# Optimization experiments

Hardware: AMD Instinct MI355X
Metric: run time of the kernel (lower is better)

Reference implementation:

```python
import jax, jax.numpy as jnp
import numpy as np

V = 20000; FV = 2000; PV = 31
SE = 400; FE = 50; PE = 5; NE = 5
FR = FE + PE + NE  # 60, field_rep_embed_size
H = 512; HH = H // 2  # decoder hidden, encoder per-direction hidden
B = 32; T = 32; S = 100
TE = 300  # target_lookup dim (hardcoded in module)


def setup_inputs() -> dict:
    key = jax.random.key(0)
    ks = jax.random.split(key, 26)
    g = lambda k, shape, s: (jax.random.normal(k, shape, jnp.float32) * s)
    inp = {}
    inp['sent'] = jax.random.randint(ks[0], (B, T), 0, V)
    inp['value'] = jax.random.randint(ks[1], (B, S), 0, V)
    inp['field'] = jax.random.randint(ks[2], (B, S), 0, FV)
    inp['ppos'] = jax.random.randint(ks[3], (B, S), 0, PV)
    inp['pneg'] = jax.random.randint(ks[4], (B, S), 0, PV)
    inp['batch_size'] = B
    inp['value_mask'] = jnp.ones((B, S), jnp.float32)
    inp['align_prob'] = jax.random.uniform(ks[5], (B, S, V), jnp.float32)
    # embedding tables
    inp['sent_emb'] = g(ks[6], (V, SE), 0.05)
    inp['field_emb'] = g(ks[7], (FV, FE), 0.05)
    inp['ppos_emb'] = g(ks[8], (PV, PE), 0.05)
    inp['pneg_emb'] = g(ks[9], (PV, NE), 0.05)
    inp['target_emb'] = g(ks[10], (V, TE), 0.05)
    # bidirectional encoder LSTM (per-direction hidden HH), torch gate order i,f,g,o
    ein = SE + FR
    inp['Wi_f'] = g(ks[11], (ein, 4 * HH), ein ** -0.5)
    inp['Wh_f'] = g(ks[12], (HH, 4 * HH), HH ** -0.5)
    inp['b_f'] = jnp.zeros((4 * HH,), jnp.float32)
    inp['Wi_b'] = g(ks[13], (ein, 4 * HH), ein ** -0.5)
    inp['Wh_b'] = g(ks[14], (HH, 4 * HH), HH ** -0.5)
    inp['b_b'] = jnp.zeros((4 * HH,), jnp.float32)
    # decoder LSTM cell + dual attention params
    inp['Wi_d'] = g(ks[15], (SE, 4 * H), SE ** -0.5)
    inp['Wh_d'] = g(ks[16], (H, 4 * H), H ** -0.5)
    inp['b_d'] = jnp.zeros((4 * H,), jnp.float32)
    inp['Wa'] = g(ks[17], (H, H), H ** -0.5)   # encoder-state attention proj
    inp['Wf'] = g(ks[18], (FR, H), FR ** -0.5) # field-rep attention proj
    inp['Wo'] = g(ks[19], (2 * H, H), (2 * H) ** -0.5)  # output proj [h;ctx]
    inp['Wl'] = g(ks[20], (2 * H + SE, 1), (2 * H + SE) ** -0.5)  # lamda gate
    inp['bl'] = jnp.zeros((1,), jnp.float32)
    # linear_out: encoder_hidden_size -> vocab
    inp['Wout'] = g(ks[21], (H, V), H ** -0.5)
    inp['bout'] = jnp.zeros((V,), jnp.float32)
    return inp


def _cell(x, h, c, Wi, Wh, b):
    z = x @ Wi + h @ Wh + b
    i, f, g, o = jnp.split(z, 4, axis=-1)
    c = jax.nn.sigmoid(f) * c + jax.nn.sigmoid(i) * jnp.tanh(g)
    h = jax.nn.sigmoid(o) * jnp.tanh(c)
    return h, c


def _run_lstm(xseq, Wi, Wh, b):
    # xseq [B,L,E] -> hs [B,L,Hn], (hT, cT)
    Bn = xseq.shape[0]; Hn = Wh.shape[0]
    init = (jnp.zeros((Bn, Hn), xseq.dtype), jnp.zeros((Bn, Hn), xseq.dtype))
    def step(carry, xt):
        h, c = _cell(xt, carry[0], carry[1], Wi, Wh, b)
        return (h, c), h
    (hT, cT), hs = jax.lax.scan(step, init, jnp.swapaxes(xseq, 0, 1))
    return jnp.swapaxes(hs, 0, 1), hT, cT


def reference(sent, value, field, ppos, pneg, batch_size, value_mask, align_prob,
              sent_emb, field_emb, ppos_emb, pneg_emb, target_emb,
              Wi_f, Wh_f, b_f, Wi_b, Wh_b, b_b,
              Wi_d, Wh_d, b_d, Wa, Wf, Wo, Wl, bl, Wout, bout):
    # --- encoder input: word emb of table values + field/pos/neg-pos embs ---
    input_d = sent_emb[value]                                     # [B,S,SE]
    input_z = jnp.concatenate([field_emb[field], ppos_emb[ppos], pneg_emb[pneg]], axis=2)  # [B,S,FR]
    enc_in = jnp.concatenate([input_d, input_z], axis=2)          # [B,S,SE+FR]
    # bidirectional LSTM (dropout is eval-mode identity)
    hs_f, hTf, cTf = _run_lstm(enc_in, Wi_f, Wh_f, b_f)
    hs_b, hTb, cTb = _run_lstm(enc_in[:, ::-1], Wi_b, Wh_b, b_b)
    enc_out = jnp.concatenate([hs_f, hs_b[:, ::-1]], axis=-1)     # [B,S,H]
    h0 = jnp.concatenate([hTf, hTb], axis=-1)                     # [B,H]
    c0 = jnp.concatenate([cTf, cTb], axis=-1)

    # --- dual-attention decoder ---
    x_seq = sent_emb[sent]                                        # [B,T,SE]
    enc_proj = jnp.einsum('bsh,hk->bsk', enc_out, Wa)             # word-level keys
    z_proj = jnp.einsum('bsf,fk->bsk', input_z, Wf)               # field-level keys

    def dstep(carry, xt):
        h, c = _cell(xt, carry[0], carry[1], Wi_d, Wh_d, b_d)
        alpha = jax.nn.softmax(jnp.einsum('bsh,bh->bs', enc_proj, h), axis=-1)
        beta = jax.nn.softmax(jnp.einsum('bsh,bh->bs', z_proj, h), axis=-1)
        g = alpha * beta
        g = g / (jnp.sum(g, axis=-1, keepdims=True) + 1e-9)       # dual attn weights
        ctx = jnp.einsum('bs,bsh->bh', g, enc_out)
        out = jnp.tanh(jnp.concatenate([h, ctx], axis=-1) @ Wo)   # [B,H]
        lam = jax.nn.sigmoid(jnp.concatenate([h, ctx, xt], axis=-1) @ Wl + bl)  # [B,1]
        return (h, c), (out, g, lam)

    (hT, cT), (outs, attn, lam) = jax.lax.scan(dstep, (h0, c0), jnp.swapaxes(x_seq, 0, 1))
    outs = jnp.swapaxes(outs, 0, 1)   # [B,T,H]
    attn = jnp.swapaxes(attn, 0, 1)   # [B,T,S]
    lam = jnp.swapaxes(lam, 0, 1)     # [B,T,1]

    p_mod = jax.nn.log_softmax(outs @ Wout + bout, axis=2)        # [B,T,V]
    p_lex = jnp.einsum('bts,bsv->btv', attn, align_prob)          # bmm
    p_bias = jax.nn.log_softmax(lam * p_lex + (1.0 - lam) * p_mod, axis=2)

    # position_idx_to_value: vectorized gather replacing the scalar double loop
    max_idx_attn = jnp.argmax(attn, axis=2)                       # [B,T]
    word_idx = jnp.take_along_axis(value, max_idx_attn, axis=1)   # [B,T]
    attn_pred = target_emb[word_idx]                              # [B,T,300]
    decoder_pred = target_emb[jnp.argmax(p_bias, axis=2)]         # [B,T,300]
    return p_bias, (hT, cT), attn_pred, decoder_pred
```

## Files before the change

### kernel.cpp

```cpp
#include <hip/hip_runtime.h>
#include <cstdint>
#include <cstddef>

static constexpr int Bn  = 32;
static constexpr int Tn  = 32;
static constexpr int Sn  = 100;
static constexpr int Vn  = 20000;
static constexpr int SEn = 400;
static constexpr int EINn= 460;
static constexpr int Hn  = 512;
static constexpr int HHn = 256;
static constexpr int TEn = 300;

__device__ __forceinline__ float sigm(float x) { return 1.f / (1.f + expf(-x)); }

__device__ __forceinline__ void fma4(float hk, const float4 w,
                                     float& zi, float& zf, float& zg, float& zo) {
    zi = fmaf(hk, w.x, zi); zf = fmaf(hk, w.y, zf);
    zg = fmaf(hk, w.z, zg); zo = fmaf(hk, w.w, zo);
}

__device__ __forceinline__ void grid_wait(int* bar, int target) {
    while (__hip_atomic_load(bar, __ATOMIC_ACQUIRE, __HIP_MEMORY_SCOPE_AGENT) < target)
        __builtin_amdgcn_s_sleep(2);
}

__global__ __launch_bounds__(256) void embed_kernel(
    const int* __restrict__ value, const int* __restrict__ field,
    const int* __restrict__ ppos, const int* __restrict__ pneg,
    const int* __restrict__ sent,
    const float* __restrict__ sent_emb, const float* __restrict__ field_emb,
    const float* __restrict__ ppos_emb, const float* __restrict__ pneg_emb,
    float* __restrict__ enc_in, float* __restrict__ x_seq)
{
    int i = blockIdx.x * 256 + threadIdx.x;
    const int total1 = Bn * Sn * EINn;
    if (i < total1) {
        int e = i % EINn, bs = i / EINn;
        float v;
        if (e < SEn)      v = sent_emb[(size_t)value[bs] * SEn + e];
        else if (e < 450) v = field_emb[field[bs] * 50 + (e - 400)];
        else if (e < 455) v = ppos_emb[ppos[bs] * 5 + (e - 450)];
        else              v = pneg_emb[pneg[bs] * 5 + (e - 455)];
        enc_in[i] = v;
    } else {
        int i2 = i - total1;
        if (i2 < Bn * Tn * SEn) {
            int e = i2 % SEn, bt = i2 / SEn;
            x_seq[i2] = sent_emb[(size_t)sent[bt] * SEn + e];
        }
    }
}

__global__ __launch_bounds__(256) void transpose_wh_kernel(
    const float* __restrict__ Whf, const float* __restrict__ Whb,
    const float* __restrict__ Whd,
    float* __restrict__ Whf_t, float* __restrict__ Whb_t, float* __restrict__ Whd_t)
{
    int i = blockIdx.x * 256 + threadIdx.x;
    if (i < 65536) {
        int k = i >> 8, u = i & 255;
        const float* p = Whf + (size_t)k * 1024 + u;
        float4 o;
        o.x = p[0]; o.y = p[256]; o.z = p[512]; o.w = p[768];
        *(float4*)(Whf_t + (size_t)i * 4) = o;
        p = Whb + (size_t)k * 1024 + u;
        o.x = p[0]; o.y = p[256]; o.z = p[512]; o.w = p[768];
        *(float4*)(Whb_t + (size_t)i * 4) = o;
    } else {
        int j = i - 65536;
        if (j < 262144) {
            int k = j >> 9, u = j & 511;
            const float* p = Whd + (size_t)k * 2048 + u;
            float4 o;
            o.x = p[0]; o.y = p[512]; o.z = p[1024]; o.w = p[1536];
            *(float4*)(Whd_t + (size_t)j * 4) = o;
        }
    }
}

__global__ __launch_bounds__(256) void gemm128_kernel(
    const float* __restrict__ A, const float* __restrict__ Bm,
    const float* __restrict__ bias, float* __restrict__ C,
    int M, int N, int K, int lda, int ldb, int ldc)
{
    __shared__ float As[8][128];
    __shared__ float Bs[8][128];
    const int bm = blockIdx.y * 128, bn = blockIdx.x * 128;
    const int tid = threadIdx.x;
    const int tx = tid & 15, ty = tid >> 4;
    const int row0 = ty * 8, col0 = tx * 8;
    float acc[8][8] = {};
    for (int k0 = 0; k0 < K; k0 += 8) {
        #pragma unroll
        for (int i = 0; i < 4; ++i) {
            int idx = tid + 256 * i;
            int m = idx >> 3, kk = idx & 7;
            float v = 0.f;
            if (bm + m < M && k0 + kk < K) v = A[(size_t)(bm + m) * lda + (k0 + kk)];
            As[kk][m] = v;
        }
        #pragma unroll
        for (int i = 0; i < 4; ++i) {
            int idx = tid + 256 * i;
            int kk = idx >> 7, n = idx & 127;
            float v = 0.f;
            if (k0 + kk < K && bn + n < N) v = Bm[(size_t)(k0 + kk) * ldb + (bn + n)];
            Bs[kk][n] = v;
        }
        __syncthreads();
        #pragma unroll
        for (int kk = 0; kk < 8; ++kk) {
            float a[8], b[8];
            #pragma unroll
            for (int i = 0; i < 8; ++i) a[i] = As[kk][row0 + i];
            #pragma unroll
            for (int j = 0; j < 8; ++j) b[j] = Bs[kk][col0 + j];
            #pragma unroll
            for (int i = 0; i < 8; ++i)
                #pragma unroll
                for (int j = 0; j < 8; ++j) acc[i][j] = fmaf(a[i], b[j], acc[i][j]);
        }
        __syncthreads();
    }
    #pragma unroll
    for (int i = 0; i < 8; ++i) {
        int m = bm + row0 + i;
        if (m >= M) continue;
        #pragma unroll
        for (int j = 0; j < 8; ++j) {
            int n = bn + col0 + j;
            if (n < N) {
                float v = acc[i][j];
                if (bias) v += bias[n];
                C[(size_t)m * ldc + n] = v;
            }
        }
    }
}

__global__ __launch_bounds__(256, 1) void enc_lstm5_kernel(
    const float* __restrict__ Xf, const float* __restrict__ Xb,
    const float4* __restrict__ Whf_t, const float4* __restrict__ Whb_t,
    float* __restrict__ enc_out, float* __restrict__ h0t, float* __restrict__ c0t,
    float* __restrict__ hbuf, int* __restrict__ bar)
{
    const int bb  = blockIdx.x;
    const int dir = bb >> 5;
    const int U0  = (bb & 31) * 8;
    const float*  __restrict__ X = dir ? Xb : Xf;
    const float4* __restrict__ W = dir ? Whb_t : Whf_t;
    float* hb = hbuf + dir * 16384;
    const int tid = threadIdx.x;
    const int b = tid & 31, uu = tid >> 5;
    const int unit = U0 + uu;
    const float4* __restrict__ wcol = W + unit;
    __shared__ float h_lds[HHn * 32];
    float c = 0.f;

    for (int s = 0; s < Sn; ++s) {
        const int src_s = dir ? (Sn - 1 - s) : s;
        const float* xr = X + ((size_t)(b * Sn + src_s)) * 1024 + unit;
        float zi = xr[0], zf = xr[256], zg = xr[512], zo = xr[768];
        if (s > 0) {
            if (tid == 0) grid_wait(bar, 64 * s);
            __syncthreads();
            const float4* src4 = (const float4*)(hb + ((s - 1) & 1) * 8192);
            float4* dst4 = (float4*)h_lds;
            #pragma unroll
            for (int i = 0; i < 8; ++i)
                dst4[tid + i * 256] = src4[tid + i * 256];
            __syncthreads();
            #pragma unroll 8
            for (int k = 0; k < 256; ++k)
                fma4(h_lds[k * 32 + b], wcol[(size_t)k * 256], zi, zf, zg, zo);
        }
        c = sigm(zf) * c + sigm(zi) * tanhf(zg);
        const float h = sigm(zo) * tanhf(c);
        enc_out[((size_t)(b * Sn + src_s)) * Hn + dir * HHn + unit] = h;
        if (s == Sn - 1) {
            h0t[(dir * HHn + unit) * 32 + b] = h;
            c0t[(dir * HHn + unit) * 32 + b] = c;
        } else {
            hb[(s & 1) * 8192 + unit * 32 + b] = h;
            __syncthreads();
            if (tid == 0)
                __hip_atomic_fetch_add(bar, 1, __ATOMIC_ACQ_REL, __HIP_MEMORY_SCOPE_AGENT);
        }
    }
}

__global__ __launch_bounds__(256, 1) void dec_lstm5_kernel(
    const float* __restrict__ Xd, const float4* __restrict__ Whd_t,
    const float* __restrict__ h0t, const float* __restrict__ c0t,
    float* __restrict__ h_all, float* __restrict__ hT, float* __restrict__ cT,
    float* __restrict__ hbuf, int* __restrict__ bar)
{
    const int U0 = blockIdx.x * 8;
    const int tid = threadIdx.x;
    const int b = tid & 31, uu = tid >> 5;
    const int unit = U0 + uu;
    const float4* __restrict__ wcol = Whd_t + unit;
    __shared__ float h_lds[Hn * 32];
    float c = c0t[unit * 32 + b];

    for (int t = 0; t < Tn; ++t) {
        const float* xr = Xd + ((size_t)(b * Tn + t)) * 2048 + unit;
        float zi = xr[0], zf = xr[512], zg = xr[1024], zo = xr[1536];
        if (t > 0) {
            if (tid == 0) grid_wait(bar, 64 * t);
        }
        __syncthreads();
        const float4* src4 = (t == 0) ? (const float4*)h0t
                                      : (const float4*)(hbuf + ((t - 1) & 1) * 16384);
        float4* dst4 = (float4*)h_lds;
        #pragma unroll
        for (int i = 0; i < 16; ++i)
            dst4[tid + i * 256] = src4[tid + i * 256];
        __syncthreads();
        #pragma unroll 8
        for (int k = 0; k < 512; ++k)
            fma4(h_lds[k * 32 + b], wcol[(size_t)k * 512], zi, zf, zg, zo);
        c = sigm(zf) * c + sigm(zi) * tanhf(zg);
        const float h = sigm(zo) * tanhf(c);
        h_all[((size_t)(b * Tn + t)) * Hn + unit] = h;
        if (t == Tn - 1) {
            hT[b * Hn + unit] = h;
            cT[b * Hn + unit] = c;
        } else {
            hbuf[(t & 1) * 16384 + unit * 32 + b] = h;
            __syncthreads();
            if (tid == 0)
                __hip_atomic_fetch_add(bar, 1, __ATOMIC_ACQ_REL, __HIP_MEMORY_SCOPE_AGENT);
        }
    }
}

__global__ __launch_bounds__(256) void dec_post_kernel(
    const float* __restrict__ h_all, const float* __restrict__ enc_proj,
    const float* __restrict__ z_proj, const float* __restrict__ enc_out,
    const float* __restrict__ x_seq, const float* __restrict__ Wo,
    const float* __restrict__ Wl, const float* __restrict__ bl,
    const int* __restrict__ value, const float* __restrict__ target_emb,
    float* __restrict__ outs, float* __restrict__ gattn,
    float* __restrict__ lamv, float* __restrict__ attn_pred)
{
    const int bt = blockIdx.x, b = bt >> 5;
    const int tid = threadIdx.x;
    __shared__ float h_sh[Hn];
    __shared__ float sc[2 * Sn];
    __shared__ float g_sh[Sn];
    __shared__ float ctx_sh[Hn];
    __shared__ float red[256];
    __shared__ int smax_sh;

    for (int i = tid; i < Hn; i += 256) h_sh[i] = h_all[(size_t)bt * Hn + i];
    __syncthreads();

    const int wave = tid >> 6, lane = tid & 63;
    for (int s = wave; s < Sn; s += 4) {
        const float* ep = enc_proj + ((size_t)b * Sn + s) * Hn;
        const float* zp = z_proj  + ((size_t)b * Sn + s) * Hn;
        float da = 0.f, db = 0.f;
        for (int j = lane; j < Hn; j += 64) {
            float hv = h_sh[j];
            da = fmaf(ep[j], hv, da);
            db = fmaf(zp[j], hv, db);
        }
        #pragma unroll
        for (int off = 32; off; off >>= 1) {
            da += __shfl_down(da, off);
            db += __shfl_down(db, off);
        }
        if (lane == 0) { sc[s] = da; sc[Sn + s] = db; }
    }
    __syncthreads();

    if (tid == 0) {
        float ma = -1e30f, mb = -1e30f;
        for (int s = 0; s < Sn; ++s) { ma = fmaxf(ma, sc[s]); mb = fmaxf(mb, sc[Sn + s]); }
        float sa = 0.f, sb = 0.f;
        for (int s = 0; s < Sn; ++s) {
            float ea = expf(sc[s] - ma), eb = expf(sc[Sn + s] - mb);
            sc[s] = ea; sc[Sn + s] = eb; sa += ea; sb += eb;
        }
        float gs = 0.f;
        for (int s = 0; s < Sn; ++s) { float g = (sc[s] / sa) * (sc[Sn + s] / sb); g_sh[s] = g; gs += g; }
        float inv = 1.f / (gs + 1e-9f);
        float best = -1.f; int bi = 0;
        for (int s = 0; s < Sn; ++s) {
            float g = g_sh[s] * inv; g_sh[s] = g;
            if (g > best) { best = g; bi = s; }
        }
        smax_sh = bi;
    }
    __syncthreads();

    for (int s = tid; s < Sn; s += 256) gattn[(size_t)bt * Sn + s] = g_sh[s];
    const int word = value[b * Sn + smax_sh];
    for (int e = tid; e < TEn; e += 256)
        attn_pred[(size_t)bt * TEn + e] = target_emb[(size_t)word * TEn + e];

    for (int u = tid; u < Hn; u += 256) {
        float acc = 0.f;
        for (int s = 0; s < Sn; ++s)
            acc = fmaf(g_sh[s], enc_out[((size_t)b * Sn + s) * Hn + u], acc);
        ctx_sh[u] = acc;
    }
    __syncthreads();

    for (int j = tid; j < Hn; j += 256) {
        float acc = 0.f;
        for (int k = 0; k < Hn; ++k) acc = fmaf(h_sh[k], Wo[(size_t)k * Hn + j], acc);
        for (int k = 0; k < Hn; ++k) acc = fmaf(ctx_sh[k], Wo[(size_t)(Hn + k) * Hn + j], acc);
        outs[(size_t)bt * Hn + j] = tanhf(acc);
    }

    float part = 0.f;
    for (int k = tid; k < Hn; k += 256) part = fmaf(h_sh[k], Wl[k], part);
    for (int k = tid; k < Hn; k += 256) part = fmaf(ctx_sh[k], Wl[Hn + k], part);
    const float* xr = x_seq + (size_t)bt * SEn;
    for (int k = tid; k < SEn; k += 256) part = fmaf(xr[k], Wl[2 * Hn + k], part);
    red[tid] = part;
    __syncthreads();
    for (int s2 = 128; s2; s2 >>= 1) {
        if (tid < s2) red[tid] += red[tid + s2];
        __syncthreads();
    }
    if (tid == 0) lamv[bt] = 1.f / (1.f + expf(-(red[0] + bl[0])));
}

__global__ __launch_bounds__(256) void p_lex_kernel(
    const float* __restrict__ gattn, const float* __restrict__ align_prob,
    float* __restrict__ p_lex)
{
    const int b = blockIdx.z, th = blockIdx.y, vc = blockIdx.x;
    const int tid = threadIdx.x;
    __shared__ float gT[Sn][17];
    for (int i = tid; i < Sn * 16; i += 256) {
        int s = i >> 4, tt = i & 15;
        gT[s][tt] = gattn[((size_t)(b * Tn + th * 16 + tt)) * Sn + s];
    }
    __syncthreads();
    const int v0 = vc * 1024 + tid * 4;
    if (v0 >= Vn) return;
    float acc[16][4] = {};
    for (int s = 0; s < Sn; ++s) {
        const float4 a = *(const float4*)(align_prob + ((size_t)b * Sn + s) * Vn + v0);
        #pragma unroll
        for (int tt = 0; tt < 16; ++tt) {
            float g = gT[s][tt];
            acc[tt][0] = fmaf(g, a.x, acc[tt][0]);
            acc[tt][1] = fmaf(g, a.y, acc[tt][1]);
            acc[tt][2] = fmaf(g, a.z, acc[tt][2]);
            acc[tt][3] = fmaf(g, a.w, acc[tt][3]);
        }
    }
    #pragma unroll
    for (int tt = 0; tt < 16; ++tt) {
        float4 o;
        o.x = acc[tt][0]; o.y = acc[tt][1]; o.z = acc[tt][2]; o.w = acc[tt][3];
        *(float4*)(p_lex + ((size_t)(b * Tn + th * 16 + tt)) * Vn + v0) = o;
    }
}

__global__ __launch_bounds__(256) void reduce1_kernel(
    const float* __restrict__ z, float* __restrict__ lse1)
{
    const int r = blockIdx.x, tid = threadIdx.x;
    const float* row = z + (size_t)r * Vn;
    __shared__ float red[256];
    float m = -1e30f;
    for (int v = tid; v < Vn; v += 256) m = fmaxf(m, row[v]);
    red[tid] = m; __syncthreads();
    for (int s = 128; s; s >>= 1) { if (tid < s) red[tid] = fmaxf(red[tid], red[tid + s]); __syncthreads(); }
    m = red[0]; __syncthreads();
    float sum = 0.f;
    for (int v = tid; v < Vn; v += 256) sum += expf(row[v] - m);
    red[tid] = sum; __syncthreads();
    for (int s = 128; s; s >>= 1) { if (tid < s) red[tid] += red[tid + s]; __syncthreads(); }
    if (tid == 0) lse1[r] = m + logf(red[0]);
}

__global__ __launch_bounds__(256) void combine_kernel(
    float* __restrict__ q, const float* __restrict__ p_lex,
    const float* __restrict__ lamv, const float* __restrict__ lse1,
    float* __restrict__ lse2, int* __restrict__ amax)
{
    const int r = blockIdx.x, tid = threadIdx.x;
    const float l = lamv[r], ls1 = lse1[r];
    float* row = q + (size_t)r * Vn;
    const float* pl = p_lex + (size_t)r * Vn;
    __shared__ float rm[256];
    __shared__ int ri[256];
    float m = -1e30f; int mi = 0;
    for (int v = tid; v < Vn; v += 256) {
        float qq = l * pl[v] + (1.f - l) * (row[v] - ls1);
        row[v] = qq;
        if (qq > m) { m = qq; mi = v; }
    }
    rm[tid] = m; ri[tid] = mi; __syncthreads();
    for (int s = 128; s; s >>= 1) {
        if (tid < s) {
            if (rm[tid + s] > rm[tid] || (rm[tid + s] == rm[tid] && ri[tid + s] < ri[tid])) {
                rm[tid] = rm[tid + s]; ri[tid] = ri[tid + s];
            }
        }
        __syncthreads();
    }
    m = rm[0];
    const int best = ri[0];
    __syncthreads();
    float sum = 0.f;
    for (int v = tid; v < Vn; v += 256) sum += expf(row[v] - m);
    rm[tid] = sum; __syncthreads();
    for (int s = 128; s; s >>= 1) { if (tid < s) rm[tid] += rm[tid + s]; __syncthreads(); }
    if (tid == 0) { lse2[r] = m + logf(rm[0]); amax[r] = best; }
}

__global__ __launch_bounds__(256) void finalize_kernel(
    float* __restrict__ pbias, const float* __restrict__ lse2,
    const int* __restrict__ amax, const float* __restrict__ target_emb,
    float* __restrict__ dec_pred)
{
    const int r = blockIdx.x, tid = threadIdx.x;
    const float ls = lse2[r];
    float* row = pbias + (size_t)r * Vn;
    for (int v = tid; v < Vn; v += 256) row[v] -= ls;
    const int wd = amax[r];
    for (int e = tid; e < TEn; e += 256)
        dec_pred[(size_t)r * TEn + e] = target_emb[(size_t)wd * TEn + e];
}

extern "C" void kernel_launch(void* const* d_in, const int* in_sizes, int n_in,
                              void* d_out, int out_size, void* d_ws, size_t ws_size,
                              hipStream_t stream)
{
    const int*   sent       = (const int*)d_in[0];
    const int*   value      = (const int*)d_in[1];
    const int*   field      = (const int*)d_in[2];
    const int*   ppos       = (const int*)d_in[3];
    const int*   pneg       = (const int*)d_in[4];
    const float* align_prob = (const float*)d_in[7];
    const float* sent_emb   = (const float*)d_in[8];
    const float* field_emb  = (const float*)d_in[9];
    const float* ppos_emb   = (const float*)d_in[10];
    const float* pneg_emb   = (const float*)d_in[11];
    const float* target_emb = (const float*)d_in[12];
    const float* Wi_f = (const float*)d_in[13];
    const float* Wh_f = (const float*)d_in[14];
    const float* b_f  = (const float*)d_in[15];
    const float* Wi_b = (const float*)d_in[16];
    const float* Wh_b = (const float*)d_in[17];
    const float* b_b  = (const float*)d_in[18];
    const float* Wi_d = (const float*)d_in[19];
    const float* Wh_d = (const float*)d_in[20];
    const float* b_d  = (const float*)d_in[21];
    const float* Wa   = (const float*)d_in[22];
    const float* Wf   = (const float*)d_in[23];
    const float* Wo   = (const float*)d_in[24];
    const float* Wl   = (const float*)d_in[25];
    const float* bl   = (const float*)d_in[26];
    const float* Wout = (const float*)d_in[27];
    const float* bout = (const float*)d_in[28];

    float* w = (float*)d_ws;
    float* enc_in   = w; w += (size_t)Bn * Sn * EINn;
    float* x_seq    = w; w += (size_t)Bn * Tn * SEn;
    float* Xf       = w; w += (size_t)Bn * Sn * 1024;
    float* Xb       = w; w += (size_t)Bn * Sn * 1024;
    float* Xd       = w; w += (size_t)Bn * Tn * 2048;
    float* enc_out  = w; w += (size_t)Bn * Sn * Hn;
    float* enc_proj = w; w += (size_t)Bn * Sn * Hn;
    float* z_proj   = w; w += (size_t)Bn * Sn * Hn;
    float* h0t      = w; w += (size_t)Bn * Hn;
    float* c0t      = w; w += (size_t)Bn * Hn;
    float* h_all    = w; w += (size_t)Bn * Tn * Hn;
    float* outs     = w; w += (size_t)Bn * Tn * Hn;
    float* gattn    = w; w += (size_t)Bn * Tn * Sn;
    float* lamv     = w; w += (size_t)Bn * Tn;
    float* p_lex    = w; w += (size_t)Bn * Tn * Vn;
    float* lse1     = w; w += (size_t)Bn * Tn;
    float* lse2     = w; w += (size_t)Bn * Tn;
    int*   amax     = (int*)w;

    float* Whf_t  = p_lex;
    float* Whb_t  = p_lex + 262144;
    float* Whd_t  = p_lex + 524288;
    float* hbuf_d = p_lex + 1600000;
    float* hbuf_e = p_lex + 1700000;
    int*   bar_e  = (int*)(p_lex + 1800000);
    int*   bar_d  = bar_e + 64;

    float* outp      = (float*)d_out;
    float* pbias     = outp;
    float* hT        = outp + (size_t)20480000;
    float* cT        = hT + Bn * Hn;
    float* attn_pred = cT + Bn * Hn;
    float* dec_pred  = attn_pred + (size_t)Bn * Tn * TEn;

    const float4* Whf_t4 = (const float4*)Whf_t;
    const float4* Whb_t4 = (const float4*)Whb_t;
    const float4* Whd_t4 = (const float4*)Whd_t;

    embed_kernel<<<7350, 256, 0, stream>>>(value, field, ppos, pneg, sent,
        sent_emb, field_emb, ppos_emb, pneg_emb, enc_in, x_seq);
    transpose_wh_kernel<<<1280, 256, 0, stream>>>(Wh_f, Wh_b, Wh_d, Whf_t, Whb_t, Whd_t);
    hipMemsetAsync(bar_e, 0, 512, stream);

    dim3 gXf(8, 25);
    gemm128_kernel<<<gXf, 256, 0, stream>>>(enc_in, Wi_f, b_f, Xf, 3200, 1024, 460, 460, 1024, 1024);
    gemm128_kernel<<<gXf, 256, 0, stream>>>(enc_in, Wi_b, b_b, Xb, 3200, 1024, 460, 460, 1024, 1024);
    dim3 gXd(16, 8);
    gemm128_kernel<<<gXd, 256, 0, stream>>>(x_seq, Wi_d, b_d, Xd, 1024, 2048, 400, 400, 2048, 2048);

    {
        void* args[] = { (void*)&Xf, (void*)&Xb, (void*)&Whf_t4, (void*)&Whb_t4,
                         (void*)&enc_out, (void*)&h0t, (void*)&c0t,
                         (void*)&hbuf_e, (void*)&bar_e };
        hipLaunchCooperativeKernel((const void*)enc_lstm5_kernel,
                                   dim3(64), dim3(256), args, 0, stream);
    }

    dim3 gPr(4, 25);
    gemm128_kernel<<<gPr, 256, 0, stream>>>(enc_out, Wa, nullptr, enc_proj, 3200, 512, 512, 512, 512, 512);
    gemm128_kernel<<<gPr, 256, 0, stream>>>(enc_in + 400, Wf, nullptr, z_proj, 3200, 512, 60, 460, 512, 512);

    {
        void* args[] = { (void*)&Xd, (void*)&Whd_t4, (void*)&h0t, (void*)&c0t,
                         (void*)&h_all, (void*)&hT, (void*)&cT,
                         (void*)&hbuf_d, (void*)&bar_d };
        hipLaunchCooperativeKernel((const void*)dec_lstm5_kernel,
                                   dim3(64), dim3(256), args, 0, stream);
    }

    dec_post_kernel<<<1024, 256, 0, stream>>>(h_all, enc_proj, z_proj, enc_out, x_seq,
        Wo, Wl, bl, value, target_emb, outs, gattn, lamv, attn_pred);

    dim3 gBig(157, 8);
    gemm128_kernel<<<gBig, 256, 0, stream>>>(outs, Wout, bout, pbias, 1024, 20000, 512, 512, 20000, 20000);

    dim3 gPl(20, 2, 32);
    p_lex_kernel<<<gPl, 256, 0, stream>>>(gattn, align_prob, p_lex);

    reduce1_kernel<<<1024, 256, 0, stream>>>(pbias, lse1);
    combine_kernel<<<1024, 256, 0, stream>>>(pbias, p_lex, lamv, lse1, lse2, amax);
    finalize_kernel<<<1024, 256, 0, stream>>>(pbias, lse2, amax, target_emb, dec_pred);

    (void)in_sizes; (void)n_in; (void)out_size; (void)ws_size;
}
```

Measured before the change: 4.346 ms.

## Replace grid-synchronized encoder LSTM with per-batch blocks and relax decoder barrier ordering

The encoder LSTM no longer splits hidden units across 64 cooperatively launched blocks that meet at a global atomic barrier every timestep. Each block now owns one (batch, direction) pair and keeps h in shared memory, so the only per-step synchronisation is __syncthreads. The cost is that every block streams the full 256x1024 recurrent weight matrix from L2 at each step. The decoder barrier switches to a relaxed spin-load, atomic loads of the shared h buffer and a release-only increment, which removes acquire/acq_rel overhead but depends on these weaker memory semantics still being correct.

```diff
diff --git a/kernel.cpp b/kernel.cpp
--- a/kernel.cpp
+++ b/kernel.cpp
@@ -18,11 +18,6 @@
                                      float& zi, float& zf, float& zg, float& zo) {
     zi = fmaf(hk, w.x, zi); zf = fmaf(hk, w.y, zf);
     zg = fmaf(hk, w.z, zg); zo = fmaf(hk, w.w, zo);
-}
-
-__device__ __forceinline__ void grid_wait(int* bar, int target) {
-    while (__hip_atomic_load(bar, __ATOMIC_ACQUIRE, __HIP_MEMORY_SCOPE_AGENT) < target)
-        __builtin_amdgcn_s_sleep(2);
 }
 
 __global__ __launch_bounds__(256) void embed_kernel(
@@ -139,58 +134,49 @@
     }
 }
 
-__global__ __launch_bounds__(256, 1) void enc_lstm5_kernel(
+__global__ __launch_bounds__(256) void enc_lstm2_kernel(
     const float* __restrict__ Xf, const float* __restrict__ Xb,
     const float4* __restrict__ Whf_t, const float4* __restrict__ Whb_t,
-    float* __restrict__ enc_out, float* __restrict__ h0t, float* __restrict__ c0t,
-    float* __restrict__ hbuf, int* __restrict__ bar)
-{
-    const int bb  = blockIdx.x;
-    const int dir = bb >> 5;
-    const int U0  = (bb & 31) * 8;
-    const float*  __restrict__ X = dir ? Xb : Xf;
+    float* __restrict__ enc_out, float* __restrict__ h0t, float* __restrict__ c0t)
+{
+    const int b = blockIdx.x >> 1, dir = blockIdx.x & 1;
+    const float* __restrict__ X = dir ? Xb : Xf;
     const float4* __restrict__ W = dir ? Whb_t : Whf_t;
-    float* hb = hbuf + dir * 16384;
-    const int tid = threadIdx.x;
-    const int b = tid & 31, uu = tid >> 5;
-    const int unit = U0 + uu;
-    const float4* __restrict__ wcol = W + unit;
-    __shared__ float h_lds[HHn * 32];
+    __shared__ __align__(16) float h_sh[HHn];
+    const int u = threadIdx.x;
     float c = 0.f;
-
-    for (int s = 0; s < Sn; ++s) {
-        const int src_s = dir ? (Sn - 1 - s) : s;
-        const float* xr = X + ((size_t)(b * Sn + src_s)) * 1024 + unit;
-        float zi = xr[0], zf = xr[256], zg = xr[512], zo = xr[768];
-        if (s > 0) {
-            if (tid == 0) grid_wait(bar, 64 * s);
-            __syncthreads();
-            const float4* src4 = (const float4*)(hb + ((s - 1) & 1) * 8192);
-            float4* dst4 = (float4*)h_lds;
-            #pragma unroll
-            for (int i = 0; i < 8; ++i)
-                dst4[tid + i * 256] = src4[tid + i * 256];
-            __syncthreads();
-            #pragma unroll 8
-            for (int k = 0; k < 256; ++k)
-                fma4(h_lds[k * 32 + b], wcol[(size_t)k * 256], zi, zf, zg, zo);
+    h_sh[u] = 0.f;
+    __syncthreads();
+    for (int step = 0; step < Sn; ++step) {
+        const int s = dir ? (Sn - 1 - step) : step;
+        const float* xr = X + ((size_t)(b * Sn + s)) * 1024;
+        float zi = xr[u], zf = xr[256 + u], zg = xr[512 + u], zo = xr[768 + u];
+        #pragma unroll 4
+        for (int k4 = 0; k4 < 64; ++k4) {
+            const float4 hv = *(const float4*)&h_sh[k4 << 2];
+            const float4 w0 = W[((k4 << 2) + 0) * 256 + u];
+            const float4 w1 = W[((k4 << 2) + 1) * 256 + u];
+            const float4 w2 = W[((k4 << 2) + 2) * 256 + u];
+            const float4 w3 = W[((k4 << 2) + 3) * 256 + u];
+            fma4(hv.x, w0, zi, zf, zg, zo);
+            fma4(hv.y, w1, zi, zf, zg, zo);
+            fma4(hv.z, w2, zi, zf, zg, zo);
+            fma4(hv.w, w3, zi, zf, zg, zo);
         }
         c = sigm(zf) * c + sigm(zi) * tanhf(zg);
-        const float h = sigm(zo) * tanhf(c);
-        enc_out[((size_t)(b * Sn + src_s)) * Hn + dir * HHn + unit] = h;
-        if (s == Sn - 1) {
-            h0t[(dir * HHn + unit) * 32 + b] = h;
-            c0t[(dir * HHn + unit) * 32 + b] = c;
-        } else {
-            hb[(s & 1) * 8192 + unit * 32 + b] = h;
-            __syncthreads();
-            if (tid == 0)
-                __hip_atomic_fetch_add(bar, 1, __ATOMIC_ACQ_REL, __HIP_MEMORY_SCOPE_AGENT);
-        }
-    }
-}
-
-__global__ __launch_bounds__(256, 1) void dec_lstm5_kernel(
+        float h = sigm(zo) * tanhf(c);
+        __syncthreads();
+        h_sh[u] = h;
+        enc_out[((size_t)(b * Sn + s)) * Hn + dir * HHn + u] = h;
+        if (step == Sn - 1) {
+            h0t[(dir * HHn + u) * 32 + b] = h;
+            c0t[(dir * HHn + u) * 32 + b] = c;
+        }
+        __syncthreads();
+    }
+}
+
+__global__ __launch_bounds__(256, 1) void dec_lstm6_kernel(
     const float* __restrict__ Xd, const float4* __restrict__ Whd_t,
     const float* __restrict__ h0t, const float* __restrict__ c0t,
     float* __restrict__ h_all, float* __restrict__ hT, float* __restrict__ cT,
@@ -207,16 +193,27 @@
     for (int t = 0; t < Tn; ++t) {
         const float* xr = Xd + ((size_t)(b * Tn + t)) * 2048 + unit;
         float zi = xr[0], zf = xr[512], zg = xr[1024], zo = xr[1536];
-        if (t > 0) {
-            if (tid == 0) grid_wait(bar, 64 * t);
-        }
-        __syncthreads();
-        const float4* src4 = (t == 0) ? (const float4*)h0t
-                                      : (const float4*)(hbuf + ((t - 1) & 1) * 16384);
-        float4* dst4 = (float4*)h_lds;
-        #pragma unroll
-        for (int i = 0; i < 16; ++i)
-            dst4[tid + i * 256] = src4[tid + i * 256];
+        if (t == 0) {
+            const float4* src4 = (const float4*)h0t;
+            float4* dst4 = (float4*)h_lds;
+            #pragma unroll
+            for (int i = 0; i < 16; ++i)
+                dst4[tid + i * 256] = src4[tid + i * 256];
+        } else {
+            if (tid == 0) {
+                while (__hip_atomic_load(bar, __ATOMIC_RELAXED,
+                                         __HIP_MEMORY_SCOPE_AGENT) < 64 * t)
+                    __builtin_amdgcn_s_sleep(2);
+            }
+            __syncthreads();
+            const unsigned long long* src8 =
+                (const unsigned long long*)(hbuf + ((t - 1) & 1) * 16384);
+            unsigned long long* dst8 = (unsigned long long*)h_lds;
+            #pragma unroll
+            for (int i = 0; i < 32; ++i)
+                dst8[tid + i * 256] = __hip_atomic_load(&src8[tid + i * 256],
+                                        __ATOMIC_RELAXED, __HIP_MEMORY_SCOPE_AGENT);
+        }
         __syncthreads();
         #pragma unroll 8
         for (int k = 0; k < 512; ++k)
@@ -231,7 +228,8 @@
             hbuf[(t & 1) * 16384 + unit * 32 + b] = h;
             __syncthreads();
             if (tid == 0)
-                __hip_atomic_fetch_add(bar, 1, __ATOMIC_ACQ_REL, __HIP_MEMORY_SCOPE_AGENT);
+                __hip_atomic_fetch_add(bar, 1, __ATOMIC_RELEASE,
+                                       __HIP_MEMORY_SCOPE_AGENT);
         }
     }
 }
@@ -488,9 +486,7 @@
     float* Whb_t  = p_lex + 262144;
     float* Whd_t  = p_lex + 524288;
     float* hbuf_d = p_lex + 1600000;
-    float* hbuf_e = p_lex + 1700000;
-    int*   bar_e  = (int*)(p_lex + 1800000);
-    int*   bar_d  = bar_e + 64;
+    int*   bar_d  = (int*)(p_lex + 1800000);
 
     float* outp      = (float*)d_out;
     float* pbias     = outp;
@@ -506,7 +502,7 @@
     embed_kernel<<<7350, 256, 0, stream>>>(value, field, ppos, pneg, sent,
         sent_emb, field_emb, ppos_emb, pneg_emb, enc_in, x_seq);
     transpose_wh_kernel<<<1280, 256, 0, stream>>>(Wh_f, Wh_b, Wh_d, Whf_t, Whb_t, Whd_t);
-    hipMemsetAsync(bar_e, 0, 512, stream);
+    hipMemsetAsync(bar_d, 0, 256, stream);
 
     dim3 gXf(8, 25);
     gemm128_kernel<<<gXf, 256, 0, stream>>>(enc_in, Wi_f, b_f, Xf, 3200, 1024, 460, 460, 1024, 1024);
@@ -514,13 +510,8 @@
     dim3 gXd(16, 8);
     gemm128_kernel<<<gXd, 256, 0, stream>>>(x_seq, Wi_d, b_d, Xd, 1024, 2048, 400, 400, 2048, 2048);
 
-    {
-        void* args[] = { (void*)&Xf, (void*)&Xb, (void*)&Whf_t4, (void*)&Whb_t4,
-                         (void*)&enc_out, (void*)&h0t, (void*)&c0t,
-                         (void*)&hbuf_e, (void*)&bar_e };
-        hipLaunchCooperativeKernel((const void*)enc_lstm5_kernel,
-                                   dim3(64), dim3(256), args, 0, stream);
-    }
+    enc_lstm2_kernel<<<64, 256, 0, stream>>>(Xf, Xb, Whf_t4, Whb_t4,
+        enc_out, h0t, c0t);
 
     dim3 gPr(4, 25);
     gemm128_kernel<<<gPr, 256, 0, stream>>>(enc_out, Wa, nullptr, enc_proj, 3200, 512, 512, 512, 512, 512);
@@ -530,7 +521,7 @@
         void* args[] = { (void*)&Xd, (void*)&Whd_t4, (void*)&h0t, (void*)&c0t,
                          (void*)&h_all, (void*)&hT, (void*)&cT,
                          (void*)&hbuf_d, (void*)&bar_d };
-        hipLaunchCooperativeKernel((const void*)dec_lstm5_kernel,
+        hipLaunchCooperativeKernel((const void*)dec_lstm6_kernel,
                                    dim3(64), dim3(256), args, 0, stream);
     }
 
```

Result: faster. 4.153 ms (-4.4%).
